# Kernel tuning notes

Hardware: AMD Instinct MI355X
Metric: run time of the kernel (lower is better)

## Reference

```python
import jax, jax.numpy as jnp
import numpy as np

B, S, IN, OUT = 4, 4096, 4096, 4096
N, R = 8, 64  # n_adapters, rank


def setup_inputs() -> dict:
    key = jax.random.key(0)
    ks = jax.random.split(key, 7)
    x = jax.random.normal(ks[0], (B, S, IN), dtype=jnp.float32)
    W = jax.random.normal(ks[1], (OUT, IN), dtype=jnp.float32) * 0.02
    b = jax.random.normal(ks[2], (OUT,), dtype=jnp.float32) * 0.02
    downs = jax.random.normal(ks[3], (N, R, IN), dtype=jnp.float32) * 0.02
    ups = jax.random.normal(ks[4], (N, OUT, R), dtype=jnp.float32) * 0.02
    mags = jax.random.uniform(ks[5], (N, OUT), dtype=jnp.float32)
    scales = jax.random.uniform(ks[6], (N,), dtype=jnp.float32)
    return {"x": x, "W": W, "b": b, "downs": downs, "ups": ups, "mags": mags, "scales": scales}


def reference(x, W, b, downs, ups, mags, scales):
    # Base linear: y = x @ W.T + b
    out = jnp.einsum("bsi,oi->bso", x, W) + b
    # All adapters batched: t[b,s,n,r] = x @ down_n.T
    t = jnp.einsum("bsi,nri->bsnr", x, downs)
    # Fold per-adapter DoRA magnitude and effective scale into the up proj:
    # delta = sum_n sc_n * mag_n * (t_n @ up_n.T)
    up_eff = ups * mags[:, :, None] * scales[:, None, None]  # [N, OUT, R]
    delta = jnp.einsum("bsnr,nor->bso", t, up_eff)
    return out + delta
```

## Files before the change

### kernel.cpp

```cpp
#include <hip/hip_runtime.h>


#define B_DIM 4
#define S_DIM 4096
#define IND   4096
#define OUTD  4096
#define NA    8
#define RK    64
#define MROWS (B_DIM * S_DIM)
#define KADAPT (NA * RK)

typedef __attribute__((ext_vector_type(8))) short short8;
typedef __attribute__((ext_vector_type(8))) unsigned short ushort8;
typedef __attribute__((ext_vector_type(4))) float float4v;

__device__ __forceinline__ unsigned short f2bf(float f) {
  unsigned int u = __builtin_bit_cast(unsigned int, f);
  u += 0x7FFFu + ((u >> 16) & 1u);
  return (unsigned short)(u >> 16);
}

__global__ void fold_up_k(const float* __restrict__ ups, const float* __restrict__ mags,
                          const float* __restrict__ scales, unsigned short* __restrict__ up_eff) {
  int tid = blockIdx.x * 256 + threadIdx.x;
  int o  = tid >> 9;
  int nr = tid & 511;
  int n  = nr >> 6;
  int r  = nr & 63;
  float v = ups[((size_t)n * OUTD + o) * RK + r] * mags[n * OUTD + o] * scales[n];
  up_eff[tid] = f2bf(v);
}

__global__ void tdown_k(const float* __restrict__ downs, unsigned short* __restrict__ dT) {
  int tid = blockIdx.x * 256 + threadIdx.x;
  int i  = tid >> 9;
  int nr = tid & 511;
  dT[tid] = f2bf(downs[(size_t)nr * IND + i]);
}

__global__ void cvt_x_k(const float* __restrict__ x, unsigned short* __restrict__ xb) {
  int tid = blockIdx.x * 256 + threadIdx.x;
  const float4v* xv = (const float4v*)x;
  float4v a = xv[2 * tid];
  float4v b = xv[2 * tid + 1];
  ushort8 o;
  o[0] = f2bf(a[0]); o[1] = f2bf(a[1]); o[2] = f2bf(a[2]); o[3] = f2bf(a[3]);
  o[4] = f2bf(b[0]); o[5] = f2bf(b[1]); o[6] = f2bf(b[2]); o[7] = f2bf(b[3]);
  ((ushort8*)xb)[tid] = o;
}

#define GLOAD_LDS16(g, l)                                                        \
  __builtin_amdgcn_global_load_lds((const __attribute__((address_space(1))) void*)(g), \
                                   (__attribute__((address_space(3))) void*)(l), 16, 0, 0)

template <int EPI>
__global__ __launch_bounds__(256) void gemm_nt(const unsigned short* __restrict__ A,
                                               const unsigned short* __restrict__ B,
                                               const float* __restrict__ extra,
                                               void* __restrict__ Cout,
                                               int M, int N, int K) {
  __shared__ __align__(16) unsigned short As[128 * 32];
  __shared__ __align__(16) unsigned short Bs[128 * 32];

  const int tid  = threadIdx.x;
  const int lane = tid & 63;
  const int w    = tid >> 6;
  const int wr   = w >> 1;
  const int wc   = w & 1;
  const int bm   = blockIdx.x;
  const int bn   = blockIdx.y;

  const int lrow = lane >> 2;
  const int lk   = (((lane & 3) ^ ((lrow >> 1) & 3))) * 8;

  const unsigned short* Abase = A + (size_t)(bm * 128) * K;
  const unsigned short* Bbase = B + (size_t)(bn * 128) * K;

  const int q    = lane >> 4;
  const int qr   = lane & 15;
  const int ks   = (q ^ ((qr >> 1) & 3)) * 8;

  float4v acc[4][4] = {};

  for (int k0 = 0; k0 < K; k0 += 32) {
#pragma unroll
    for (int s = 0; s < 2; ++s) {
      int seg = w * 2 + s;
      int row = seg * 16 + lrow;
      GLOAD_LDS16(Abase + (size_t)row * K + k0 + lk, &As[seg * 512]);
      GLOAD_LDS16(Bbase + (size_t)row * K + k0 + lk, &Bs[seg * 512]);
    }
    __syncthreads();

    short8 af[4], bfr[4];
#pragma unroll
    for (int t = 0; t < 4; ++t) {
      int arow = wr * 64 + t * 16 + qr;
      af[t] = *(const short8*)&As[arow * 32 + ks];
      int bcol = wc * 64 + t * 16 + qr;
      bfr[t] = *(const short8*)&Bs[bcol * 32 + ks];
    }
#pragma unroll
    for (int tm = 0; tm < 4; ++tm)
#pragma unroll
      for (int tn = 0; tn < 4; ++tn)
        acc[tm][tn] = __builtin_amdgcn_mfma_f32_16x16x32_bf16(af[tm], bfr[tn], acc[tm][tn], 0, 0, 0);
    __syncthreads();
  }

  if (EPI == 0) {
    float* C = (float*)Cout;
#pragma unroll
    for (int tn = 0; tn < 4; ++tn) {
      int col = bn * 128 + wc * 64 + tn * 16 + qr;
      float bias = extra[col];
#pragma unroll
      for (int tm = 0; tm < 4; ++tm) {
        int rbase = bm * 128 + wr * 64 + tm * 16 + q * 4;
#pragma unroll
        for (int r2 = 0; r2 < 4; ++r2) {
          C[(size_t)(rbase + r2) * N + col] = acc[tm][tn][r2] + bias;
        }
      }
    }
  } else {
    unsigned short* C = (unsigned short*)Cout;
#pragma unroll
    for (int tn = 0; tn < 4; ++tn) {
      int col = bn * 128 + wc * 64 + tn * 16 + qr;
#pragma unroll
      for (int tm = 0; tm < 4; ++tm) {
        int rbase = bm * 128 + wr * 64 + tm * 16 + q * 4;
#pragma unroll
        for (int r2 = 0; r2 < 4; ++r2) {
          size_t idx = (size_t)(rbase + r2) * N + col;
          C[idx] = f2bf(acc[tm][tn][r2] + extra[idx]);
        }
      }
    }
  }
}

extern "C" void kernel_launch(void* const* d_in, const int* in_sizes, int n_in,
                              void* d_out, int out_size, void* d_ws, size_t ws_size,
                              hipStream_t stream) {
  const float* x      = (const float*)d_in[0];
  const float* W      = (const float*)d_in[1];
  const float* b      = (const float*)d_in[2];
  const float* downs  = (const float*)d_in[3];
  const float* ups    = (const float*)d_in[4];
  const float* mags   = (const float*)d_in[5];
  const float* scales = (const float*)d_in[6];
  float* out = (float*)d_out;

  char* ws = (char*)d_ws;
  unsigned short* x_bf   = (unsigned short*)ws;
  unsigned short* w_eff  = (unsigned short*)(ws + 134217728ull);
  unsigned short* up_eff = (unsigned short*)(ws + 134217728ull + 33554432ull);
  unsigned short* dT     = (unsigned short*)(ws + 134217728ull + 33554432ull + 4194304ull);

  fold_up_k<<<dim3((OUTD * KADAPT) / 256), dim3(256), 0, stream>>>(ups, mags, scales, up_eff);
  tdown_k<<<dim3((IND * KADAPT) / 256), dim3(256), 0, stream>>>(downs, dT);
  cvt_x_k<<<dim3((MROWS * IND / 8) / 256), dim3(256), 0, stream>>>(x, x_bf);

  gemm_nt<1><<<dim3(OUTD / 128, IND / 128), dim3(256), 0, stream>>>(
      up_eff, dT, W, (void*)w_eff, OUTD, IND, KADAPT);

  gemm_nt<0><<<dim3(MROWS / 128, OUTD / 128), dim3(256), 0, stream>>>(
      x_bf, w_eff, b, (void*)out, MROWS, OUTD, IND);
}
```

Baseline: 1.298 ms.

## Rewrite GEMM as 256x256 tile, double-buffered LDS pipeline with XCD swizzle

Replaces the 128x128 single-buffered bf16 MFMA GEMM with a 256x256-tile, 512-thread kernel. It double-buffers K=64 stages in LDS and interleaves async global-to-LDS loads with MFMA quarters using explicit waitcnt, barriers and setprio. It also remaps workgroups in groups of 8 to improve L2 locality per XCD. The goal is to hide memory latency and raise data reuse per loaded tile, at the cost of heavy LDS use (128KB), many accumulator registers, and drop of the earlier LDS swizzle, which may cause bank conflicts.

```diff
diff --git a/kernel.cpp b/kernel.cpp
--- a/kernel.cpp
+++ b/kernel.cpp
@@ -54,91 +54,179 @@
                                    (__attribute__((address_space(3))) void*)(l), 16, 0, 0)
 
 template <int EPI>
-__global__ __launch_bounds__(256) void gemm_nt(const unsigned short* __restrict__ A,
-                                               const unsigned short* __restrict__ B,
-                                               const float* __restrict__ extra,
-                                               void* __restrict__ Cout,
-                                               int M, int N, int K) {
-  __shared__ __align__(16) unsigned short As[128 * 32];
-  __shared__ __align__(16) unsigned short Bs[128 * 32];
+__global__ __launch_bounds__(512, 2) void gemm256(const unsigned short* __restrict__ A,
+                                                  const unsigned short* __restrict__ B,
+                                                  const float* __restrict__ extra,
+                                                  void* __restrict__ Cout,
+                                                  int M, int N, int K) {
+  __shared__ __align__(16) unsigned short As[2][2][256 * 32];
+  __shared__ __align__(16) unsigned short Bs[2][2][256 * 32];
 
   const int tid  = threadIdx.x;
   const int lane = tid & 63;
   const int w    = tid >> 6;
-  const int wr   = w >> 1;
-  const int wc   = w & 1;
-  const int bm   = blockIdx.x;
-  const int bn   = blockIdx.y;
-
-  const int lrow = lane >> 2;
-  const int lk   = (((lane & 3) ^ ((lrow >> 1) & 3))) * 8;
-
-  const unsigned short* Abase = A + (size_t)(bm * 128) * K;
-  const unsigned short* Bbase = B + (size_t)(bn * 128) * K;
-
-  const int q    = lane >> 4;
+  const int wm   = w >> 2;
+  const int wn   = w & 3;
   const int qr   = lane & 15;
-  const int ks   = (q ^ ((qr >> 1) & 3)) * 8;
-
-  float4v acc[4][4] = {};
-
-  for (int k0 = 0; k0 < K; k0 += 32) {
-#pragma unroll
-    for (int s = 0; s < 2; ++s) {
-      int seg = w * 2 + s;
-      int row = seg * 16 + lrow;
-      GLOAD_LDS16(Abase + (size_t)row * K + k0 + lk, &As[seg * 512]);
-      GLOAD_LDS16(Bbase + (size_t)row * K + k0 + lk, &Bs[seg * 512]);
-    }
-    __syncthreads();
-
-    short8 af[4], bfr[4];
-#pragma unroll
-    for (int t = 0; t < 4; ++t) {
-      int arow = wr * 64 + t * 16 + qr;
-      af[t] = *(const short8*)&As[arow * 32 + ks];
-      int bcol = wc * 64 + t * 16 + qr;
-      bfr[t] = *(const short8*)&Bs[bcol * 32 + ks];
-    }
-#pragma unroll
-    for (int tm = 0; tm < 4; ++tm)
-#pragma unroll
-      for (int tn = 0; tn < 4; ++tn)
-        acc[tm][tn] = __builtin_amdgcn_mfma_f32_16x16x32_bf16(af[tm], bfr[tn], acc[tm][tn], 0, 0, 0);
-    __syncthreads();
+  const int q8   = (lane >> 4) * 8;
+
+  const int nwg  = gridDim.x * gridDim.y;
+  const int orig = blockIdx.y * gridDim.x + blockIdx.x;
+  const int cpx  = nwg >> 3;
+  const int swz  = (orig & 7) * cpx + (orig >> 3);
+  const int bm   = swz / gridDim.y;
+  const int bn   = swz % gridDim.y;
+
+  const size_t Kz = (size_t)K;
+  const unsigned short* aSrc = A + ((size_t)bm * 256 + w * 32 + (lane >> 2)) * Kz + (lane & 3) * 8;
+  const unsigned short* bSrc = B + ((size_t)bn * 256 + w * 32 + (lane >> 2)) * Kz + (lane & 3) * 8;
+  const size_t seg1 = 16 * Kz;
+
+  unsigned short* aBuf = &As[0][0][0];
+  unsigned short* bBuf = &Bs[0][0][0];
+
+#define STAGE(SRC, REG)                                 \
+  do {                                                  \
+    GLOAD_LDS16((SRC), (REG) + w * 1024);               \
+    GLOAD_LDS16((SRC) + seg1, (REG) + w * 1024 + 512);  \
+  } while (0)
+
+#define LDS_A(REG, MH)                                                                    \
+  {                                                                                       \
+    _Pragma("unroll") for (int fm = 0; fm < 4; ++fm)                                      \
+      a[fm] = *(const short8*)((REG) + (wm * 128 + ((MH) * 4 + fm) * 16 + qr) * 32 + q8); \
+  }
+
+#define LDS_B(REG)                                                                        \
+  {                                                                                       \
+    _Pragma("unroll") for (int fn = 0; fn < 4; ++fn)                                      \
+      b[fn] = *(const short8*)((REG) + (wn * 64 + fn * 16 + qr) * 32 + q8);               \
+  }
+
+#define MFMA_Q(MH)                                                                        \
+  __builtin_amdgcn_sched_barrier(0);                                                      \
+  __builtin_amdgcn_s_barrier();                                                           \
+  asm volatile("s_waitcnt lgkmcnt(0)" ::: "memory");                                      \
+  __builtin_amdgcn_sched_barrier(0);                                                      \
+  __builtin_amdgcn_s_setprio(1);                                                          \
+  {                                                                                       \
+    _Pragma("unroll") for (int fm = 0; fm < 4; ++fm)                                      \
+      _Pragma("unroll") for (int fn = 0; fn < 4; ++fn)                                    \
+        acc[(MH) * 4 + fm][fn] = __builtin_amdgcn_mfma_f32_16x16x32_bf16(                 \
+            a[fm], b[fn], acc[(MH) * 4 + fm][fn], 0, 0, 0);                               \
+  }                                                                                       \
+  __builtin_amdgcn_s_setprio(0);                                                          \
+  __builtin_amdgcn_sched_barrier(0);
+
+  float4v acc[8][4] = {};
+  short8 a[4], b[4];
+
+  const int NT = K >> 6;
+
+  STAGE(aSrc, aBuf);
+  STAGE(bSrc, bBuf);
+  STAGE(aSrc + 32, aBuf + 8192);
+  STAGE(bSrc + 32, bBuf + 8192);
+  asm volatile("s_waitcnt vmcnt(4)" ::: "memory");
+  __builtin_amdgcn_s_barrier();
+
+  for (int t = 0; t < NT - 1; ++t) {
+    const int pc = (t & 1) << 14;
+    const int pn = pc ^ 16384;
+    unsigned short* aCur = aBuf + pc;
+    unsigned short* bCur = bBuf + pc;
+    unsigned short* aNx  = aBuf + pn;
+    unsigned short* bNx  = bBuf + pn;
+    const unsigned short* aN = aSrc + 64;
+    const unsigned short* bN = bSrc + 64;
+
+    LDS_A(aCur, 0);
+    LDS_B(bCur);
+    STAGE(aN, aNx);
+    MFMA_Q(0);
+    __builtin_amdgcn_s_barrier();
+
+    LDS_A(aCur, 1);
+    STAGE(bN, bNx);
+    MFMA_Q(1);
+    asm volatile("s_waitcnt vmcnt(4)" ::: "memory");
+    __builtin_amdgcn_s_barrier();
+
+    LDS_A(aCur + 8192, 0);
+    LDS_B(bCur + 8192);
+    STAGE(aN + 32, aNx + 8192);
+    MFMA_Q(0);
+    __builtin_amdgcn_s_barrier();
+
+    LDS_A(aCur + 8192, 1);
+    STAGE(bN + 32, bNx + 8192);
+    MFMA_Q(1);
+    asm volatile("s_waitcnt vmcnt(4)" ::: "memory");
+    __builtin_amdgcn_s_barrier();
+
+    aSrc = aN;
+    bSrc = bN;
+  }
+
+  {
+    const int pc = ((NT - 1) & 1) << 14;
+    unsigned short* aCur = aBuf + pc;
+    unsigned short* bCur = bBuf + pc;
+
+    LDS_A(aCur, 0);
+    LDS_B(bCur);
+    MFMA_Q(0);
+    __builtin_amdgcn_s_barrier();
+
+    LDS_A(aCur, 1);
+    MFMA_Q(1);
+    asm volatile("s_waitcnt vmcnt(0)" ::: "memory");
+    __builtin_amdgcn_s_barrier();
+
+    LDS_A(aCur + 8192, 0);
+    LDS_B(bCur + 8192);
+    MFMA_Q(0);
+    __builtin_amdgcn_s_barrier();
+
+    LDS_A(aCur + 8192, 1);
+    MFMA_Q(1);
   }
 
   if (EPI == 0) {
     float* C = (float*)Cout;
 #pragma unroll
-    for (int tn = 0; tn < 4; ++tn) {
-      int col = bn * 128 + wc * 64 + tn * 16 + qr;
-      float bias = extra[col];
-#pragma unroll
-      for (int tm = 0; tm < 4; ++tm) {
-        int rbase = bm * 128 + wr * 64 + tm * 16 + q * 4;
-#pragma unroll
-        for (int r2 = 0; r2 < 4; ++r2) {
-          C[(size_t)(rbase + r2) * N + col] = acc[tm][tn][r2] + bias;
-        }
+    for (int fn = 0; fn < 4; ++fn) {
+      const int col = bn * 256 + wn * 64 + fn * 16 + qr;
+      const float bias = extra[col];
+#pragma unroll
+      for (int fm = 0; fm < 8; ++fm) {
+        const int rbase = bm * 256 + wm * 128 + fm * 16 + (lane >> 4) * 4;
+#pragma unroll
+        for (int r2 = 0; r2 < 4; ++r2)
+          C[(size_t)(rbase + r2) * N + col] = acc[fm][fn][r2] + bias;
       }
     }
   } else {
     unsigned short* C = (unsigned short*)Cout;
 #pragma unroll
-    for (int tn = 0; tn < 4; ++tn) {
-      int col = bn * 128 + wc * 64 + tn * 16 + qr;
-#pragma unroll
-      for (int tm = 0; tm < 4; ++tm) {
-        int rbase = bm * 128 + wr * 64 + tm * 16 + q * 4;
+    for (int fn = 0; fn < 4; ++fn) {
+      const int col = bn * 256 + wn * 64 + fn * 16 + qr;
+#pragma unroll
+      for (int fm = 0; fm < 8; ++fm) {
+        const int rbase = bm * 256 + wm * 128 + fm * 16 + (lane >> 4) * 4;
 #pragma unroll
         for (int r2 = 0; r2 < 4; ++r2) {
-          size_t idx = (size_t)(rbase + r2) * N + col;
-          C[idx] = f2bf(acc[tm][tn][r2] + extra[idx]);
+          const size_t idx = (size_t)(rbase + r2) * N + col;
+          C[idx] = f2bf(acc[fm][fn][r2] + extra[idx]);
         }
       }
     }
   }
+
+#undef STAGE
+#undef LDS_A
+#undef LDS_B
+#undef MFMA_Q
 }
 
 extern "C" void kernel_launch(void* const* d_in, const int* in_sizes, int n_in,
@@ -163,9 +251,9 @@
   tdown_k<<<dim3((IND * KADAPT) / 256), dim3(256), 0, stream>>>(downs, dT);
   cvt_x_k<<<dim3((MROWS * IND / 8) / 256), dim3(256), 0, stream>>>(x, x_bf);
 
-  gemm_nt<1><<<dim3(OUTD / 128, IND / 128), dim3(256), 0, stream>>>(
+  gemm256<1><<<dim3(OUTD / 256, IND / 256), dim3(512), 0, stream>>>(
       up_eff, dT, W, (void*)w_eff, OUTD, IND, KADAPT);
 
-  gemm_nt<0><<<dim3(MROWS / 128, OUTD / 128), dim3(256), 0, stream>>>(
+  gemm256<0><<<dim3(MROWS / 256, OUTD / 256), dim3(512), 0, stream>>>(
       x_bf, w_eff, b, (void*)out, MROWS, OUTD, IND);
 }
```

After: 1.231 ms. -5.1%, faster.
